# Performance work log

Hardware: AMD Instinct MI355X
Metric: run time of the kernel (lower is better)

## Reference

```python
import jax, jax.numpy as jnp
import numpy as np

BETA = 0.25


def setup_inputs() -> dict:
    key = jax.random.key(0)
    k1, k2, k3 = jax.random.split(key, 3)
    B, T, D, K = 4, 2048, 512, 16384
    z_e = jax.random.normal(k1, (B, T, D), dtype=jnp.float32)
    codebook = jax.random.normal(k2, (K, D), dtype=jnp.float32)  # frozen embedding
    # nn.Linear(D, D, bias=False) weight, scaled like kaiming-uniform magnitude
    W = jax.random.normal(k3, (D, D), dtype=jnp.float32) * (1.0 / np.sqrt(D))
    return {"z_e": z_e, "codebook": codebook, "W": W}


def reference(z_e, codebook, W):
    B, T, D = z_e.shape
    # effective codebook: Linear(codebook) = codebook @ W.T   -> (K, D)
    eff = jnp.matmul(codebook, W.T)
    z_flat = z_e.reshape(-1, D)  # (N, D)
    # squared euclidean distances (argmin-equivalent to cdist p=2)
    d2 = (
        jnp.sum(z_flat * z_flat, axis=1, keepdims=True)  # (N,1)
        - 2.0 * jnp.matmul(z_flat, eff.T)                  # (N,K)
        + jnp.sum(eff * eff, axis=1)[None, :]              # (1,K)
    )
    code_indices = jnp.argmin(d2, axis=1)  # (N,)
    z_q = eff[code_indices].reshape(B, T, D)
    loss_w = jnp.mean((jax.lax.stop_gradient(z_e) - z_q) ** 2)
    loss_commit = BETA * jnp.mean((z_e - jax.lax.stop_gradient(z_q)) ** 2)
    total_loss = loss_w + loss_commit
    # straight-through estimator
    z_q_out = z_e + jax.lax.stop_gradient(z_q - z_e)
    return z_q_out, total_loss, code_indices.reshape(B, T)
```

## Files before the change

### kernel.cpp

```cpp
#include <hip/hip_runtime.h>
#include <stdint.h>


#define N_ROWS 8192
#define DIM    512
#define K_CB   16384
#define TILE_F16 16384
#define HALF_F16 8192
#define KT_EFF 24
#define KT_D   8
#define TILE_P8 16384
#define HALF_P8 8192
#define PAN_P8  ((size_t)KT_D * TILE_P8)
#define RMARGIN 28.0f
#define TMARG   0.5f
#define MAXC    256

typedef _Float16 f16x8 __attribute__((ext_vector_type(8)));
typedef float f32x4 __attribute__((ext_vector_type(4)));
typedef long lx2 __attribute__((ext_vector_type(2)));

#define FENCE() asm volatile("" ::: "memory")
#define BARRIER() do { FENCE(); __builtin_amdgcn_s_barrier(); FENCE(); } while (0)
#define VMCNT(n) asm volatile("s_waitcnt vmcnt(" #n ")" ::: "memory")

__device__ __forceinline__ void gload_lds16(const void* g, void* l) {
  __builtin_amdgcn_global_load_lds(
      (const __attribute__((address_space(1))) uint32_t*)g,
      (__attribute__((address_space(3))) uint32_t*)l, 16, 0, 0);
}

__device__ __forceinline__ unsigned cvt2_fp8(float a, float b) {
  unsigned r;
  asm("v_cvt_pk_fp8_f32 %0, %1, %2" : "=v"(r) : "v"(a), "v"(b));
  return r & 0xFFFFu;
}

__global__ __launch_bounds__(256) void split_tiled_kernel(
    const float* __restrict__ S, _Float16* __restrict__ T, int resid_limb) {
  const int b = blockIdx.x;
  const int mp = b / 48;
  const int r1 = b % 48;
  const int kt = r1 >> 1, half = r1 & 1;
  const int limb = kt >> 3;
  const int ksrc = (kt & 7) * 64;
  const bool resid = (limb == resid_limb);
  const int t = threadIdx.x;
  _Float16* dst = T + ((size_t)(mp * KT_EFF + kt) * 2 + half) * HALF_F16;
#pragma unroll
  for (int cc = 0; cc < 4; ++cc) {
    const int ci = cc * 256 + t;
    const int kblk = ci >> 7, row = ci & 127;
    const int m = mp * 256 + half * 128 + row;
    const float* src = &S[(size_t)m * DIM + ksrc + kblk * 8];
    float4 x0 = *reinterpret_cast<const float4*>(src);
    float4 x1 = *reinterpret_cast<const float4*>(src + 4);
    const float xs[8] = {x0.x, x0.y, x0.z, x0.w, x1.x, x1.y, x1.z, x1.w};
    f16x8 o;
    if (!resid) {
#pragma unroll
      for (int j = 0; j < 8; ++j) o[j] = (_Float16)xs[j];
    } else {
#pragma unroll
      for (int j = 0; j < 8; ++j) {
        _Float16 h = (_Float16)xs[j];
        o[j] = (_Float16)(xs[j] - (float)h);
      }
    }
    *reinterpret_cast<f16x8*>(&dst[(size_t)ci * 8]) = o;
  }
}

__global__ __launch_bounds__(256) void split1_kernel(
    const float* __restrict__ S, uint8_t* __restrict__ T) {
  const int b = blockIdx.x;
  const int p = b >> 4;
  const int r1 = b & 15;
  const int kt = r1 >> 1, half = r1 & 1;
  const int ksrc = kt * 64;
  const int t = threadIdx.x;
  uint8_t* dst = T + ((size_t)(p * KT_D + kt) * 2 + half) * HALF_P8;
#pragma unroll
  for (int cc = 0; cc < 4; ++cc) {
    const int ci = cc * 256 + t;
    const int kblk = ci >> 7, row = ci & 127;
    const int m = p * 256 + half * 128 + row;
    const float* src = &S[(size_t)m * DIM + ksrc + kblk * 8];
    float4 x0 = *reinterpret_cast<const float4*>(src);
    float4 x1 = *reinterpret_cast<const float4*>(src + 4);
    const unsigned lo = cvt2_fp8(x0.x, x0.y) | (cvt2_fp8(x0.z, x0.w) << 16);
    const unsigned hi = cvt2_fp8(x1.x, x1.y) | (cvt2_fp8(x1.z, x1.w) << 16);
    const uint64_t pack = (uint64_t)lo | ((uint64_t)hi << 32);
    const int q = kblk & 3, h2 = kblk >> 2;
    *reinterpret_cast<uint64_t*>(&dst[(size_t)(q * 128 + row) * 16 + h2 * 8]) =
        pack;
  }
}

__global__ __launch_bounds__(256) void effgemm128_kernel(
    const _Float16* __restrict__ CpT, const _Float16* __restrict__ WpT,
    float* __restrict__ eff, uint8_t* __restrict__ BpT) {
  __shared__ __align__(16) _Float16 lbuf[2][2][HALF_F16];
  const int tid = threadIdx.x;
  const int w = tid >> 6, lane = tid & 63;
  const int lh = lane & 15, lq = lane >> 4;
  const int wr = w >> 1, wc = w & 1;
  const int bid = blockIdx.x;
  const int nb = bid & 3, mh = bid >> 2;
  const int pA = mh >> 1, hA = mh & 1;
  const int pB = nb >> 1, hB = nb & 1;
  f32x4 acc[4][4] = {};

  auto stage = [&](int kt, int buf) {
    const _Float16* a = CpT + (((size_t)pA * KT_EFF + kt) * 2 + hA) * HALF_F16;
    const _Float16* b = WpT + (((size_t)pB * KT_EFF + kt) * 2 + hB) * HALF_F16;
#pragma unroll
    for (int i = 0; i < 4; ++i) {
      const int off = i * 2048 + w * 512;
      gload_lds16(a + off + lane * 8, &lbuf[buf][0][off]);
      gload_lds16(b + off + lane * 8, &lbuf[buf][1][off]);
    }
  };

  stage(0, 0);
  for (int kt = 0; kt < KT_EFF; ++kt) {
    __syncthreads();
    if (kt + 1 < KT_EFF) stage(kt + 1, (kt + 1) & 1);
    const _Float16* At = &lbuf[kt & 1][0][0];
    const _Float16* Bt = &lbuf[kt & 1][1][0];
    f16x8 af[4][2], bf[4][2];
#pragma unroll
    for (int mf = 0; mf < 4; ++mf) {
      const int r = wr * 64 + mf * 16 + lh;
#pragma unroll
      for (int kk = 0; kk < 2; ++kk)
        af[mf][kk] = *reinterpret_cast<const f16x8*>(
            &At[((kk * 4 + lq) * 128 + r) * 8]);
    }
#pragma unroll
    for (int nf = 0; nf < 4; ++nf) {
      const int r = wc * 64 + nf * 16 + lh;
#pragma unroll
      for (int kk = 0; kk < 2; ++kk)
        bf[nf][kk] = *reinterpret_cast<const f16x8*>(
            &Bt[((kk * 4 + lq) * 128 + r) * 8]);
    }
    __builtin_amdgcn_s_setprio(1);
#pragma unroll
    for (int kk = 0; kk < 2; ++kk)
#pragma unroll
      for (int mf = 0; mf < 4; ++mf)
#pragma unroll
        for (int nf = 0; nf < 4; ++nf)
          acc[mf][nf] = __builtin_amdgcn_mfma_f32_16x16x32_f16(
              af[mf][kk], bf[nf][kk], acc[mf][nf], 0, 0, 0);
    __builtin_amdgcn_s_setprio(0);
  }

#pragma unroll
  for (int mf = 0; mf < 4; ++mf)
#pragma unroll
    for (int nf = 0; nf < 4; ++nf) {
      const int cl = wc * 64 + nf * 16 + lh;
      const int col = nb * 128 + cl;
      const int ktd = col >> 6, kd = col & 63;
      const int q = (kd >> 3) & 3, h2 = kd >> 5, jb = kd & 7;
      const unsigned c01 = cvt2_fp8(acc[mf][nf][0], acc[mf][nf][1]);
      const unsigned c23 = cvt2_fp8(acc[mf][nf][2], acc[mf][nf][3]);
#pragma unroll
      for (int j = 0; j < 4; ++j) {
        const int rl = wr * 64 + mf * 16 + lq * 4 + j;
        const int row = mh * 128 + rl;
        eff[(size_t)row * DIM + col] = acc[mf][nf][j];
        const unsigned byte =
            (j < 2 ? (c01 >> (j * 8)) : (c23 >> ((j - 2) * 8))) & 255u;
        BpT[((((size_t)(row >> 8) * KT_D + ktd) * 2 + ((row >> 7) & 1)) * 4 + q)
                * 2048 + (row & 127) * 16 + h2 * 8 + jb] = (uint8_t)byte;
      }
    }
}

__global__ __launch_bounds__(256) void eff16_kernel(
    const float* __restrict__ E, _Float16* __restrict__ E16) {
  const size_t base = ((size_t)blockIdx.x * 256 + threadIdx.x) * 16;
  const float4* s = (const float4*)(E + base);
  const float4 a = s[0], b = s[1], c = s[2], d = s[3];
  f16x8 lo, hi;
  lo[0] = (_Float16)a.x; lo[1] = (_Float16)a.y;
  lo[2] = (_Float16)a.z; lo[3] = (_Float16)a.w;
  lo[4] = (_Float16)b.x; lo[5] = (_Float16)b.y;
  lo[6] = (_Float16)b.z; lo[7] = (_Float16)b.w;
  hi[0] = (_Float16)c.x; hi[1] = (_Float16)c.y;
  hi[2] = (_Float16)c.z; hi[3] = (_Float16)c.w;
  hi[4] = (_Float16)d.x; hi[5] = (_Float16)d.y;
  hi[6] = (_Float16)d.z; hi[7] = (_Float16)d.w;
  *reinterpret_cast<f16x8*>(E16 + base) = lo;
  *reinterpret_cast<f16x8*>(E16 + base + 8) = hi;
}

__global__ __launch_bounds__(256) void effnorm_kernel(
    const float* __restrict__ E, float* __restrict__ En) {
  const int w = threadIdx.x >> 6;
  const int lane = threadIdx.x & 63;
  const int row = blockIdx.x * 4 + w;
  const float* er = &E[(size_t)row * DIM];
  float s = 0.f;
#pragma unroll
  for (int k = 0; k < DIM / 64; ++k) {
    float v = er[lane + k * 64];
    s = fmaf(v, v, s);
  }
#pragma unroll
  for (int o = 32; o; o >>= 1) s += __shfl_down(s, o, 64);
  if (lane == 0) En[row] = s;
}


__device__ __forceinline__ void stage_half8(const uint8_t* src, uint8_t* ldsb,
                                            int tid) {
  gload_lds16(src + tid * 16, ldsb + tid * 16);
}

template <int MQ>
__device__ __forceinline__ void read_a8(const uint8_t* At, int wr, int lh, int lq,
                                        lx2 af[4]) {
#pragma unroll
  for (int m2 = 0; m2 < 4; ++m2) {
    const int row = wr * 128 + (MQ * 4 + m2) * 16 + lh;
    const int half = row >> 7, r = row & 127;
    af[m2] = *reinterpret_cast<const lx2*>(
        &At[(size_t)half * 8192 + (lq * 128 + r) * 16]);
  }
}

template <int NQ>
__device__ __forceinline__ void read_b8(const uint8_t* Bt, int wc, int lh, int lq,
                                        lx2 bf[4]) {
#pragma unroll
  for (int n2 = 0; n2 < 2; ++n2) {
    const int row = wc * 64 + (NQ * 2 + n2) * 16 + lh;
    const int half = row >> 7, r = row & 127;
    bf[NQ * 2 + n2] = *reinterpret_cast<const lx2*>(
        &Bt[(size_t)half * 8192 + (lq * 128 + r) * 16]);
  }
}

template <int MQ, int NQ>
__device__ __forceinline__ void mfma_phase8(const lx2 af[4], const lx2 bf[4],
                                            f32x4 acc[8][4]) {
  __builtin_amdgcn_s_setprio(1);
#pragma unroll
  for (int kk = 0; kk < 2; ++kk)
#pragma unroll
    for (int m2 = 0; m2 < 4; ++m2)
#pragma unroll
      for (int n2 = 0; n2 < 2; ++n2)
        acc[MQ * 4 + m2][NQ * 2 + n2] = __builtin_amdgcn_mfma_f32_16x16x32_fp8_fp8(
            af[m2][kk], bf[NQ * 2 + n2][kk], acc[MQ * 4 + m2][NQ * 2 + n2], 0, 0, 0);
  __builtin_amdgcn_s_setprio(0);
}

__device__ __forceinline__ void pipeline8_p8(
    const uint8_t* Ab, const uint8_t* Bb, uint8_t (&lds)[4][TILE_P8],
    f32x4 (&acc)[8][4], int tid, int wr, int wc, int lh, int lq, int NT) {
  lx2 af[4], bf[4];
  stage_half8(Ab, &lds[0][0], tid);
  stage_half8(Ab + HALF_P8, &lds[0][HALF_P8], tid);
  stage_half8(Bb, &lds[1][0], tid);
  stage_half8(Bb + HALF_P8, &lds[1][HALF_P8], tid);
  stage_half8(Bb + TILE_P8, &lds[3][0], tid);
  stage_half8(Bb + TILE_P8 + HALF_P8, &lds[3][HALF_P8], tid);
  stage_half8(Ab + TILE_P8, &lds[2][0], tid);
  VMCNT(3);
  BARRIER();
  for (int t = 0; t < NT; ++t) {
    const int s = t & 1;
    const uint8_t* At = &lds[s * 2 + 0][0];
    const uint8_t* Bt = &lds[s * 2 + 1][0];
    read_a8<0>(At, wr, lh, lq, af);
    read_b8<0>(Bt, wc, lh, lq, bf);
    if (t + 1 < NT)
      stage_half8(Ab + (size_t)(t + 1) * TILE_P8 + HALF_P8,
                  &lds[(s ^ 1) * 2][HALF_P8], tid);
    BARRIER();
    mfma_phase8<0, 0>(af, bf, acc);
    BARRIER();
    read_b8<1>(Bt, wc, lh, lq, bf);
    BARRIER();
    mfma_phase8<0, 1>(af, bf, acc);
    BARRIER();
    read_a8<1>(At, wr, lh, lq, af);
    if (t + 2 < NT)
      stage_half8(Bb + (size_t)(t + 2) * TILE_P8, &lds[s * 2 + 1][0], tid);
    BARRIER();
    mfma_phase8<1, 1>(af, bf, acc);
    BARRIER();
    if (t + 2 < NT) {
      stage_half8(Bb + (size_t)(t + 2) * TILE_P8 + HALF_P8,
                  &lds[s * 2 + 1][HALF_P8], tid);
      stage_half8(Ab + (size_t)(t + 2) * TILE_P8, &lds[s * 2][0], tid);
    }
    BARRIER();
    mfma_phase8<1, 0>(af, bf, acc);
    if (t == NT - 2) { VMCNT(0); } else { VMCNT(3); }
    BARRIER();
  }
}

__global__ __launch_bounds__(512) void dist1_kernel(
    const uint8_t* __restrict__ ApT, const uint8_t* __restrict__ BpT,
    const float* __restrict__ En, float* __restrict__ gv,
    unsigned* __restrict__ gmask) {
  __shared__ __align__(16) uint8_t lds[4][TILE_P8];
  const int tid = threadIdx.x;
  const int w = tid >> 6, lane = tid & 63;
  const int lh = lane & 15, lq = lane >> 4;
  const int wr = w >> 2, wc = w & 3;
  const int bid = blockIdx.x;
  const int xcd = bid & 7, c = bid >> 3;
  const int np = xcd * 8 + (c & 7);
  const int mp = c >> 3;
  f32x4 acc[8][4] = {};
  pipeline8_p8(ApT + (size_t)mp * PAN_P8, BpT + (size_t)np * PAN_P8, lds, acc,
               tid, wr, wc, lh, lq, KT_D);
  float en[4];
#pragma unroll
  for (int nf = 0; nf < 4; ++nf)
    en[nf] = En[np * 256 + wc * 64 + nf * 16 + lh];
#pragma unroll
  for (int mf = 0; mf < 8; ++mf) {
#pragma unroll
    for (int j = 0; j < 4; ++j) {
      const float s0 = fmaf(-2.f, acc[mf][0][j], en[0]);
      const float s1 = fmaf(-2.f, acc[mf][1][j], en[1]);
      const float s2 = fmaf(-2.f, acc[mf][2][j], en[2]);
      const float s3 = fmaf(-2.f, acc[mf][3][j], en[3]);
      float v0 = fminf(s0, s1);
      float v1 = fminf(s2, s3);
#pragma unroll
      for (int m = 1; m < 16; m <<= 1) {
        v0 = fminf(v0, __shfl_xor(v0, m, 64));
        v1 = fminf(v1, __shfl_xor(v1, m, 64));
      }
      const unsigned long long b0 = __ballot(s0 <= v0 + RMARGIN);
      const unsigned long long b1 = __ballot(s1 <= v0 + RMARGIN);
      const unsigned long long b2 = __ballot(s2 <= v1 + RMARGIN);
      const unsigned long long b3 = __ballot(s3 <= v1 + RMARGIN);
      if (lh == 0) {
        const int row = mp * 256 + wr * 128 + mf * 16 + lq * 4 + j;
        const unsigned w0 = (unsigned)((b0 >> (lq * 16)) & 0xFFFFull) |
                            ((unsigned)((b1 >> (lq * 16)) & 0xFFFFull) << 16);
        const unsigned w1 = (unsigned)((b2 >> (lq * 16)) & 0xFFFFull) |
                            ((unsigned)((b3 >> (lq * 16)) & 0xFFFFull) << 16);
        float2* gp = (float2*)&gv[(size_t)row * 512 + np * 8 + wc * 2];
        *gp = make_float2(v0, v1);
        uint2* mq = (uint2*)&gmask[(size_t)row * 512 + np * 8 + wc * 2];
        *mq = make_uint2(w0, w1);
      }
    }
  }
}

__global__ __launch_bounds__(256) void refine_kernel(
    const float* __restrict__ Z, const float* __restrict__ E,
    const _Float16* __restrict__ E16, const float* __restrict__ En,
    const float* __restrict__ gv, const unsigned* __restrict__ gmask,
    float* __restrict__ zq, float* __restrict__ out_idx,
    float* __restrict__ ploss) {
  const int w = threadIdx.x >> 6;
  const int row = blockIdx.x * 4 + w;
  const int lane = threadIdx.x & 63;
  const int hl = lane & 31;
  const int hi = lane >> 5;
  __shared__ float ss[4][MAXC];
  __shared__ int sc[4][MAXC];

  float v[8];
#pragma unroll
  for (int i = 0; i < 8; ++i) v[i] = gv[(size_t)row * 512 + i * 64 + lane];
  float A = fminf(fminf(fminf(v[0], v[1]), fminf(v[2], v[3])),
                  fminf(fminf(v[4], v[5]), fminf(v[6], v[7])));
#pragma unroll
  for (int m = 1; m < 64; m <<= 1) A = fminf(A, __shfl_xor(A, m, 64));
  const float thr = A + RMARGIN;

  float4 zr0, zr1, zr2, zr3;
  {
    const float4* zp = (const float4*)(Z + (size_t)row * 512 + hl * 16);
    zr0 = zp[0]; zr1 = zp[1]; zr2 = zp[2]; zr3 = zp[3];
  }
  const float4* z4 = (const float4*)(Z + (size_t)row * 512 + lane * 8);
  const float4 za = z4[0], zb = z4[1];

  float bv = 3.0e38f;
  int bi = 2147483647;

  auto exact64 = [&](int colu) {
    const float4* er = (const float4*)(E + (size_t)colu * 512 + lane * 8);
    const float4 ea4 = er[0], eb4 = er[1];
    float p = 0.f;
    p = fmaf(za.x, ea4.x, p); p = fmaf(za.y, ea4.y, p);
    p = fmaf(za.z, ea4.z, p); p = fmaf(za.w, ea4.w, p);
    p = fmaf(zb.x, eb4.x, p); p = fmaf(zb.y, eb4.y, p);
    p = fmaf(zb.z, eb4.z, p); p = fmaf(zb.w, eb4.w, p);
#pragma unroll
    for (int s2 = 1; s2 < 64; s2 <<= 1) p += __shfl_xor(p, s2, 64);
    const float vv = fmaf(-2.f, p, En[colu]);
    if (vv < bv || (vv == bv && colu < bi)) { bv = vv; bi = colu; }
  };

  int nc = 0;
#pragma unroll 1
  for (int i = 0; i < 8; ++i) {
    unsigned long long bm = __ballot(v[i] <= thr);
    while (bm) {
      const int l = __builtin_ctzll(bm);
      bm &= bm - 1;
      const int g = i * 64 + l;
      unsigned m = gmask[(size_t)row * 512 + g];
      while (m) {
        const int c0 = __builtin_ctz(m);
        m &= m - 1;
        int c1 = -1;
        if (m) { c1 = __builtin_ctz(m); m &= m - 1; }
        const bool act = (c1 >= 0);
        const int cl = hi ? c1 : c0;
        const int col = g * 32 + ((hi && act) ? c1 : c0);
        (void)cl;
        if (nc < MAXC - 1) {
          const f16x8 ea = *reinterpret_cast<const f16x8*>(
              E16 + (size_t)col * 512 + hl * 16);
          const f16x8 eb = *reinterpret_cast<const f16x8*>(
              E16 + (size_t)col * 512 + hl * 16 + 8);
          float p = 0.f;
          p = fmaf((float)ea[0], zr0.x, p); p = fmaf((float)ea[1], zr0.y, p);
          p = fmaf((float)ea[2], zr0.z, p); p = fmaf((float)ea[3], zr0.w, p);
          p = fmaf((float)ea[4], zr1.x, p); p = fmaf((float)ea[5], zr1.y, p);
          p = fmaf((float)ea[6], zr1.z, p); p = fmaf((float)ea[7], zr1.w, p);
          p = fmaf((float)eb[0], zr2.x, p); p = fmaf((float)eb[1], zr2.y, p);
          p = fmaf((float)eb[2], zr2.z, p); p = fmaf((float)eb[3], zr2.w, p);
          p = fmaf((float)eb[4], zr3.x, p); p = fmaf((float)eb[5], zr3.y, p);
          p = fmaf((float)eb[6], zr3.z, p); p = fmaf((float)eb[7], zr3.w, p);
#pragma unroll
          for (int s2 = 1; s2 < 32; s2 <<= 1) p += __shfl_xor(p, s2, 64);
          const float vv = fmaf(-2.f, p, En[col]);
          if (lane == 0) { ss[w][nc] = vv; sc[w][nc] = col; }
          if (lane == 32 && act) { ss[w][nc + 1] = vv; sc[w][nc + 1] = col; }
          nc += act ? 2 : 1;
        } else {
          exact64(g * 32 + c0);
          if (act) exact64(g * 32 + c1);
        }
      }
    }
  }

  float m16 = 3.0e38f;
  for (int q = lane; q < nc; q += 64) m16 = fminf(m16, ss[w][q]);
#pragma unroll
  for (int s2 = 1; s2 < 64; s2 <<= 1) m16 = fminf(m16, __shfl_xor(m16, s2, 64));
  const float thr2 = m16 + TMARG;
#pragma unroll 1
  for (int q = 0; q < nc; ++q) {
    const float sv = ss[w][q];
    if (sv <= thr2) exact64(sc[w][q]);
  }
  const int idx = bi;

  const float4* e4 = (const float4*)(E + (size_t)idx * 512 + lane * 8);
  float4* q4 = (float4*)(zq + (size_t)row * 512 + lane * 8);
  const float4 ea = e4[0], eb = e4[1];
  q4[0] = ea; q4[1] = eb;
  float s = 0.f;
  s = fmaf(za.x - ea.x, za.x - ea.x, s); s = fmaf(za.y - ea.y, za.y - ea.y, s);
  s = fmaf(za.z - ea.z, za.z - ea.z, s); s = fmaf(za.w - ea.w, za.w - ea.w, s);
  s = fmaf(zb.x - eb.x, zb.x - eb.x, s); s = fmaf(zb.y - eb.y, zb.y - eb.y, s);
  s = fmaf(zb.z - eb.z, zb.z - eb.z, s); s = fmaf(zb.w - eb.w, zb.w - eb.w, s);
#pragma unroll
  for (int o = 32; o; o >>= 1) s += __shfl_down(s, o, 64);
  if (lane == 0) {
    ploss[row] = s;
    out_idx[row] = (float)idx;
  }
}

__global__ __launch_bounds__(256) void loss_final_kernel(
    const float* __restrict__ ploss, float* __restrict__ out_loss) {
  const int t = threadIdx.x;
  double s = 0.0;
  for (int i = t; i < N_ROWS; i += 256) s += (double)ploss[i];
#pragma unroll
  for (int o = 32; o; o >>= 1) s += __shfl_down(s, o, 64);
  __shared__ double ds[4];
  if ((t & 63) == 0) ds[t >> 6] = s;
  __syncthreads();
  if (t == 0) {
    double tot = ds[0] + ds[1] + ds[2] + ds[3];
    out_loss[0] = (float)(1.25 * tot / ((double)N_ROWS * (double)DIM));
  }
}


extern "C" void kernel_launch(void* const* d_in, const int* in_sizes, int n_in,
                              void* d_out, int out_size, void* d_ws, size_t ws_size,
                              hipStream_t stream) {
  const float* z_e      = (const float*)d_in[0];
  const float* codebook = (const float*)d_in[1];
  const float* W        = (const float*)d_in[2];
  float* out = (float*)d_out;
  char* ws = (char*)d_ws;

  float*          eff     = (float*)(ws);
  float*          effnorm = (float*)(ws + 33554432);
  _Float16*       WpT     = (_Float16*)(ws + 33619968);
  float*          ploss   = (float*)(ws + 36274176);
  _Float16*       CpT     = (_Float16*)(ws + 36306944);
  float*          gv      = (float*)(ws + 36306944);
  unsigned*       gmask   = (unsigned*)(ws + 53084160);
  _Float16*       eff16   = (_Float16*)(ws + 69861376);
  uint8_t*        BpT     = (uint8_t*)(ws + 86638592);
  uint8_t*        ApT     = (uint8_t*)(ws + 95027200);

  float* out_zq   = out;
  float* out_loss = out + (size_t)N_ROWS * DIM;
  float* out_idx  = out + (size_t)N_ROWS * DIM + 1;

  split_tiled_kernel<<<64 * 48, 256, 0, stream>>>(codebook, CpT, 2);
  split_tiled_kernel<<<2 * 48, 256, 0, stream>>>(W, WpT, 1);
  effgemm128_kernel<<<512, 256, 0, stream>>>(CpT, WpT, eff, BpT);
  eff16_kernel<<<2048, 256, 0, stream>>>(eff, eff16);
  effnorm_kernel<<<K_CB / 4, 256, 0, stream>>>(eff, effnorm);
  split1_kernel<<<32 * 16, 256, 0, stream>>>(z_e, ApT);
  dist1_kernel<<<2048, 512, 0, stream>>>(ApT, BpT, effnorm, gv, gmask);
  refine_kernel<<<N_ROWS / 4, 256, 0, stream>>>(z_e, eff, eff16, effnorm, gv,
                                                gmask, out_zq, out_idx, ploss);
  loss_final_kernel<<<1, 256, 0, stream>>>(ploss, out_loss);
}
```

Baseline: 302.8 us.

## Restructure refine into group-list, candidate-list and software-pipelined fp16 scoring phases

The refine kernel now first collects the surviving 32-column groups into an LDS list, then loads their masks in parallel across lanes and expands them into a flat candidate column list. Candidates are then scored two per wave, with the fp16 row loads for the next pair prefetched while the current pair is computed, and each dot product split across two accumulators. This targets the serialized per-candidate load latency of the old interleaved loop. The list capacity grows to 384 and the exact-recheck margin widens to 1.0, which means more fp32 rechecks and more LDS use per block.

Measured after the change: 297.3 us. Within noise of the previous version (-1.8%).

```diff
diff --git a/kernel.cpp b/kernel.cpp
--- a/kernel.cpp
+++ b/kernel.cpp
@@ -13,8 +13,9 @@
 #define HALF_P8 8192
 #define PAN_P8  ((size_t)KT_D * TILE_P8)
 #define RMARGIN 28.0f
-#define TMARG   0.5f
-#define MAXC    256
+#define TMARG   1.0f
+#define MAXC    384
+#define GCAP    384
 
 typedef _Float16 f16x8 __attribute__((ext_vector_type(8)));
 typedef float f32x4 __attribute__((ext_vector_type(4)));
@@ -372,8 +373,9 @@
   const int lane = threadIdx.x & 63;
   const int hl = lane & 31;
   const int hi = lane >> 5;
+  __shared__ unsigned short gl[4][GCAP];
+  __shared__ int clist[4][MAXC];
   __shared__ float ss[4][MAXC];
-  __shared__ int sc[4][MAXC];
 
   float v[8];
 #pragma unroll
@@ -409,7 +411,7 @@
     if (vv < bv || (vv == bv && colu < bi)) { bv = vv; bi = colu; }
   };
 
-  int nc = 0;
+  int ng = 0;
 #pragma unroll 1
   for (int i = 0; i < 8; ++i) {
     unsigned long long bm = __ballot(v[i] <= thr);
@@ -417,42 +419,71 @@
       const int l = __builtin_ctzll(bm);
       bm &= bm - 1;
       const int g = i * 64 + l;
-      unsigned m = gmask[(size_t)row * 512 + g];
+      if (ng < GCAP) {
+        if (lane == 0) gl[w][ng] = (unsigned short)g;
+        ++ng;
+      } else {
+        unsigned m = gmask[(size_t)row * 512 + g];
+        while (m) { const int c = __builtin_ctz(m); m &= m - 1;
+                    exact64(g * 32 + c); }
+      }
+    }
+  }
+
+  int nc = 0;
+#pragma unroll 1
+  for (int base = 0; base < ng; base += 64) {
+    const int lim = (ng - base < 64) ? (ng - base) : 64;
+    unsigned mym = 0;
+    if (lane < lim)
+      mym = gmask[(size_t)row * 512 + gl[w][base + lane]];
+#pragma unroll 1
+    for (int j = 0; j < lim; ++j) {
+      unsigned m = (unsigned)__shfl((int)mym, j, 64);
+      const int g = gl[w][base + j];
       while (m) {
-        const int c0 = __builtin_ctz(m);
+        const int c = __builtin_ctz(m);
         m &= m - 1;
-        int c1 = -1;
-        if (m) { c1 = __builtin_ctz(m); m &= m - 1; }
-        const bool act = (c1 >= 0);
-        const int cl = hi ? c1 : c0;
-        const int col = g * 32 + ((hi && act) ? c1 : c0);
-        (void)cl;
-        if (nc < MAXC - 1) {
-          const f16x8 ea = *reinterpret_cast<const f16x8*>(
-              E16 + (size_t)col * 512 + hl * 16);
-          const f16x8 eb = *reinterpret_cast<const f16x8*>(
-              E16 + (size_t)col * 512 + hl * 16 + 8);
-          float p = 0.f;
-          p = fmaf((float)ea[0], zr0.x, p); p = fmaf((float)ea[1], zr0.y, p);
-          p = fmaf((float)ea[2], zr0.z, p); p = fmaf((float)ea[3], zr0.w, p);
-          p = fmaf((float)ea[4], zr1.x, p); p = fmaf((float)ea[5], zr1.y, p);
-          p = fmaf((float)ea[6], zr1.z, p); p = fmaf((float)ea[7], zr1.w, p);
-          p = fmaf((float)eb[0], zr2.x, p); p = fmaf((float)eb[1], zr2.y, p);
-          p = fmaf((float)eb[2], zr2.z, p); p = fmaf((float)eb[3], zr2.w, p);
-          p = fmaf((float)eb[4], zr3.x, p); p = fmaf((float)eb[5], zr3.y, p);
-          p = fmaf((float)eb[6], zr3.z, p); p = fmaf((float)eb[7], zr3.w, p);
-#pragma unroll
-          for (int s2 = 1; s2 < 32; s2 <<= 1) p += __shfl_xor(p, s2, 64);
-          const float vv = fmaf(-2.f, p, En[col]);
-          if (lane == 0) { ss[w][nc] = vv; sc[w][nc] = col; }
-          if (lane == 32 && act) { ss[w][nc + 1] = vv; sc[w][nc + 1] = col; }
-          nc += act ? 2 : 1;
+        if (nc < MAXC) {
+          if (lane == 0) clist[w][nc] = g * 32 + c;
+          ++nc;
         } else {
-          exact64(g * 32 + c0);
-          if (act) exact64(g * 32 + c1);
+          exact64(g * 32 + c);
         }
       }
     }
+  }
+
+  f16x8 a0, a1, b0, b1;
+  float en0 = 0.f, en1 = 0.f;
+  auto issue = [&](int q, f16x8& x0, f16x8& x1, float& e) {
+    int qq = q + hi;
+    if (qq > nc - 1) qq = nc - 1;
+    const int col = clist[w][qq];
+    const _Float16* ep = E16 + (size_t)col * 512 + hl * 16;
+    x0 = *reinterpret_cast<const f16x8*>(ep);
+    x1 = *reinterpret_cast<const f16x8*>(ep + 8);
+    e = En[col];
+  };
+  if (nc > 0) issue(0, a0, a1, en0);
+#pragma unroll 1
+  for (int q = 0; q < nc; q += 2) {
+    if (q + 2 < nc) issue(q + 2, b0, b1, en1);
+    float p0 = 0.f, p1 = 0.f;
+    p0 = fmaf((float)a0[0], zr0.x, p0); p1 = fmaf((float)a0[1], zr0.y, p1);
+    p0 = fmaf((float)a0[2], zr0.z, p0); p1 = fmaf((float)a0[3], zr0.w, p1);
+    p0 = fmaf((float)a0[4], zr1.x, p0); p1 = fmaf((float)a0[5], zr1.y, p1);
+    p0 = fmaf((float)a0[6], zr1.z, p0); p1 = fmaf((float)a0[7], zr1.w, p1);
+    p0 = fmaf((float)a1[0], zr2.x, p0); p1 = fmaf((float)a1[1], zr2.y, p1);
+    p0 = fmaf((float)a1[2], zr2.z, p0); p1 = fmaf((float)a1[3], zr2.w, p1);
+    p0 = fmaf((float)a1[4], zr3.x, p0); p1 = fmaf((float)a1[5], zr3.y, p1);
+    p0 = fmaf((float)a1[6], zr3.z, p0); p1 = fmaf((float)a1[7], zr3.w, p1);
+    float p = p0 + p1;
+#pragma unroll
+    for (int s2 = 1; s2 < 32; s2 <<= 1) p += __shfl_xor(p, s2, 64);
+    const float sc = fmaf(-2.f, p, en0);
+    if (hl == 0 && q + hi < nc) ss[w][q + hi] = sc;
+    a0 = b0; a1 = b1; en0 = en1;
   }
 
   float m16 = 3.0e38f;
@@ -462,8 +493,7 @@
   const float thr2 = m16 + TMARG;
 #pragma unroll 1
   for (int q = 0; q < nc; ++q) {
-    const float sv = ss[w][q];
-    if (sv <= thr2) exact64(sc[w][q]);
+    if (ss[w][q] <= thr2) exact64(clist[w][q]);
   }
   const int idx = bi;
 
```
